# Kernel optimization log

Measured on AMD Instinct MI355X. Metric: run time of the kernel, lower is better.

The kernel has to match this reference:

```python
import jax, jax.numpy as jnp
import numpy as np

B, T, D, H, O, E, K = 2, 2048, 1024, 4096, 1024, 8, 2


def setup_inputs() -> dict:
    key = jax.random.key(0)
    ks = jax.random.split(key, 10)
    s = 0.02  # small init scale to keep activations well-conditioned
    return {
        "x": jax.random.normal(ks[0], (B, T, D), jnp.float32),
        "noise": jax.random.normal(ks[1], (B, T, E), jnp.float32),
        "Wg": jax.random.normal(ks[2], (D, E), jnp.float32) * s,
        "bg": jnp.zeros((E,), jnp.float32),
        "Wn": jax.random.normal(ks[3], (D, E), jnp.float32) * s,
        "bn": jnp.zeros((E,), jnp.float32),
        "W1": jax.random.normal(ks[4], (E, D, H), jnp.float32) * s,
        "b1": jnp.zeros((E, H), jnp.float32),
        "W2": jax.random.normal(ks[5], (E, H, O), jnp.float32) * s,
        "b2": jnp.zeros((E, O), jnp.float32),
    }


def reference(x, noise, Wg, bg, Wn, bn, W1, b1, W2, b2):
    # --- NoisyTopkRouter ---
    logits = x @ Wg + bg                    # [B,T,E]
    noise_logits = x @ Wn + bn              # [B,T,E]
    noisy = logits + noise * jax.nn.softplus(noise_logits)
    top_v, top_i = jax.lax.top_k(noisy, K)  # [B,T,K]
    # scatter top-k logits into a -inf background, softmax -> sparse gates
    mask = jax.nn.one_hot(top_i, E, dtype=noisy.dtype).sum(-2)  # [B,T,E] in {0,1}
    sparse_logits = jnp.where(mask > 0, noisy, -jnp.inf)
    gating = jax.nn.softmax(sparse_logits, axis=-1)
    # mask + L1 normalize (F.normalize p=1, dim=2)
    gating = gating * mask
    gating = gating / jnp.maximum(jnp.sum(jnp.abs(gating), axis=-1, keepdims=True), 1e-12)
    # --- dense run of ALL experts (faithful to the naive torch module) ---
    h = jax.nn.relu(jnp.einsum('btd,edh->beth', x, W1) + b1[:, None, :])   # [B,E,T,H]
    expert_out = jnp.einsum('beth,eho->beto', h, W2) + b2[:, None, :]       # [B,E,T,O]
    # combine: torch transposes to [B,T,E,O] then einsum 'bte,bteo->bto'
    out = jnp.einsum('bte,beto->bto', gating, expert_out)                   # [B,T,O]
    return out
```

## Files before the change

kernel.cpp:

```cpp
#include <hip/hip_runtime.h>
#include <hip/hip_bf16.h>

#define TOK 4096
#define DD  1024
#define HH  4096
#define OO  1024
#define EE  8
#define MAX_SLOTS 80

typedef float  f32x4  __attribute__((ext_vector_type(4)));
typedef __bf16 bf16x8 __attribute__((ext_vector_type(8)));
typedef __bf16 bf16x4 __attribute__((ext_vector_type(4)));
typedef unsigned int u32x4 __attribute__((ext_vector_type(4)));

union ABCast { u32x4 u; bf16x8 b; };

typedef __attribute__((address_space(3))) unsigned int       lds_uint;
typedef const __attribute__((address_space(1))) unsigned int glob_uint;

__device__ __forceinline__ void gload_lds16(void* lds, const void* g) {
    __builtin_amdgcn_global_load_lds((glob_uint*)g, (lds_uint*)lds, 16, 0, 0);
}

__global__ void router_kernel(const float* __restrict__ x, const float* __restrict__ noise,
                              const float* __restrict__ Wg, const float* __restrict__ bg,
                              const float* __restrict__ Wn, const float* __restrict__ bn,
                              int* __restrict__ topk_e, float* __restrict__ topk_g,
                              int* __restrict__ cnt)
{
    int wave = threadIdx.x >> 6;
    int lane = threadIdx.x & 63;
    int token = blockIdx.x * 4 + wave;
    const float* xr = x + (size_t)token * DD;
    float accg[EE], accn[EE];
#pragma unroll
    for (int e = 0; e < EE; ++e) { accg[e] = 0.f; accn[e] = 0.f; }
    for (int jj = 0; jj < DD / 64; ++jj) {
        int d = lane + jj * 64;
        float xv = xr[d];
        const float* wgr = Wg + d * EE;
        const float* wnr = Wn + d * EE;
#pragma unroll
        for (int e = 0; e < EE; ++e) {
            accg[e] += xv * wgr[e];
            accn[e] += xv * wnr[e];
        }
    }
#pragma unroll
    for (int off = 32; off; off >>= 1) {
#pragma unroll
        for (int e = 0; e < EE; ++e) {
            accg[e] += __shfl_down(accg[e], off, 64);
            accn[e] += __shfl_down(accn[e], off, 64);
        }
    }
    if (lane == 0) {
        float noisy[EE];
#pragma unroll
        for (int e = 0; e < EE; ++e) {
            float lg = accg[e] + bg[e];
            float nl = accn[e] + bn[e];
            float sp = fmaxf(nl, 0.f) + log1pf(expf(-fabsf(nl)));
            noisy[e] = lg + noise[(size_t)token * EE + e] * sp;
        }
        int i1 = 0; float v1 = noisy[0];
#pragma unroll
        for (int e = 1; e < EE; ++e) if (noisy[e] > v1) { v1 = noisy[e]; i1 = e; }
        int i2 = -1; float v2 = -1e30f;
#pragma unroll
        for (int e = 0; e < EE; ++e) if (e != i1 && noisy[e] > v2) { v2 = noisy[e]; i2 = e; }
        float ex = expf(v2 - v1);
        float g1 = 1.f / (1.f + ex);
        float g2 = ex / (1.f + ex);
        topk_e[token * 2] = i1;  topk_e[token * 2 + 1] = i2;
        topk_g[token * 2] = g1;  topk_g[token * 2 + 1] = g2;
        atomicAdd(&cnt[i1], 1);
        atomicAdd(&cnt[i2], 1);
    }
}

__global__ void plan_kernel(const int* __restrict__ cnt, int* __restrict__ base_row,
                            int* __restrict__ slot_e, int* __restrict__ slot_m,
                            int* __restrict__ fill)
{
    if (threadIdx.x == 0 && blockIdx.x == 0) {
        int s = 0;
        for (int e = 0; e < EE; ++e) {
            base_row[e] = s * 128;
            int tiles = (cnt[e] + 127) >> 7;
            for (int t = 0; t < tiles; ++t) { slot_e[s] = e; slot_m[s] = t; ++s; }
            fill[e] = 0;
        }
        for (int s2 = s; s2 < MAX_SLOTS; ++s2) { slot_e[s2] = -1; slot_m[s2] = 0; }
    }
}

__global__ void scatter_kernel(const int* __restrict__ topk_e, const float* __restrict__ topk_g,
                               const int* __restrict__ base_row, int* __restrict__ fill,
                               int* __restrict__ row_token, float* __restrict__ row_gate)
{
    int t = blockIdx.x * blockDim.x + threadIdx.x;
    if (t >= TOK * 2) return;
    int e = topk_e[t];
    int pos = atomicAdd(&fill[e], 1);
    int row = base_row[e] + pos;
    row_token[row] = t >> 1;
    row_gate[row] = topk_g[t];
}

__global__ void convert_x_kernel(const float* __restrict__ in, __bf16* __restrict__ out)
{
    int i = blockIdx.x * blockDim.x + threadIdx.x;
    f32x4 v = ((const f32x4*)in)[i];
    bf16x4 o;
    o.x = (__bf16)v.x; o.y = (__bf16)v.y; o.z = (__bf16)v.z; o.w = (__bf16)v.w;
    ((bf16x4*)out)[i] = o;
}

__global__ void transpose_cvt_kernel(const float* __restrict__ in, __bf16* __restrict__ out,
                                     int R, int C)
{
    __shared__ __bf16 tile[32][33];
    int e = blockIdx.z;
    const float* ine = in + (size_t)e * R * C;
    __bf16* oute = out + (size_t)e * R * C;
    int tx = threadIdx.x & 31, ty = threadIdx.x >> 5;
    int c0 = blockIdx.x * 32, r0 = blockIdx.y * 32;
#pragma unroll
    for (int i = 0; i < 4; ++i) {
        int r = r0 + ty + i * 8;
        tile[ty + i * 8][tx] = (__bf16)ine[(size_t)r * C + c0 + tx];
    }
    __syncthreads();
#pragma unroll
    for (int i = 0; i < 4; ++i) {
        int c = c0 + ty + i * 8;
        oute[(size_t)c * R + r0 + tx] = tile[tx][ty + i * 8];
    }
}

__global__ void gemm1_kernel(const __bf16* __restrict__ xb,
                             const __bf16* __restrict__ W1t,
                             const float* __restrict__ b1bias,
                             const int* __restrict__ slot_e, const int* __restrict__ slot_m,
                             const int* __restrict__ base_row, const int* __restrict__ cnt,
                             const int* __restrict__ row_token,
                             __bf16* __restrict__ h)
{
    int slot = blockIdx.y;
    int e = slot_e[slot];
    if (e < 0) return;
    int mt = slot_m[slot];
    int row0 = base_row[e] + mt * 128;
    int rows_in = min(128, cnt[e] - mt * 128);
    int n0 = blockIdx.x * 128;

    __shared__ u32x4 Alds[512];
    __shared__ u32x4 Blds[512];

    int tid = threadIdx.x;
    int wv = tid >> 6, lane = tid & 63;

    int ar0 = tid & 127,        ak0 = tid >> 7;
    int ar1 = ar0,              ak1 = ak0 + 2;
    int tok0 = (ar0 < rows_in) ? row_token[row0 + ar0] : 0;
    const char* ag0 = (const char*)(xb + (size_t)tok0 * DD + ak0 * 8);
    const char* ag1 = (const char*)(xb + (size_t)tok0 * DD + ak1 * 8);
    const __bf16* bbase = W1t + (size_t)e * HH * DD + (size_t)n0 * DD;
    const char* bg0 = (const char*)(bbase + (size_t)ar0 * DD + ak0 * 8);
    const char* bg1 = (const char*)(bbase + (size_t)ar1 * DD + ak1 * 8);

    int wm = wv & 1, wn = wv >> 1;
    int quad = lane >> 4, l16 = lane & 15;

    f32x4 acc[4][4];
#pragma unroll
    for (int i = 0; i < 4; ++i)
#pragma unroll
        for (int j = 0; j < 4; ++j) acc[i][j] = (f32x4)(0.0f);

    for (int kb = 0; kb < DD * 2; kb += 64) {
        __syncthreads();
        gload_lds16(&Alds[wv * 64],       ag0 + kb);
        gload_lds16(&Alds[256 + wv * 64], ag1 + kb);
        gload_lds16(&Blds[wv * 64],       bg0 + kb);
        gload_lds16(&Blds[256 + wv * 64], bg1 + kb);
        __syncthreads();
        ABCast af[4], bfr[4];
#pragma unroll
        for (int mf = 0; mf < 4; ++mf) af[mf].u = Alds[quad * 128 + wm * 64 + mf * 16 + l16];
#pragma unroll
        for (int nf = 0; nf < 4; ++nf) bfr[nf].u = Blds[quad * 128 + wn * 64 + nf * 16 + l16];
#pragma unroll
        for (int mf = 0; mf < 4; ++mf)
#pragma unroll
            for (int nf = 0; nf < 4; ++nf)
                acc[mf][nf] = __builtin_amdgcn_mfma_f32_16x16x32_bf16(af[mf].b, bfr[nf].b, acc[mf][nf], 0, 0, 0);
    }

#pragma unroll
    for (int mf = 0; mf < 4; ++mf) {
        int rl = wm * 64 + mf * 16 + quad * 4;
#pragma unroll
        for (int i = 0; i < 4; ++i) {
            int rli = rl + i;
            if (rli < rows_in) {
                size_t hrow = (size_t)(row0 + rli) * HH;
#pragma unroll
                for (int nf = 0; nf < 4; ++nf) {
                    int col = n0 + wn * 64 + nf * 16 + l16;
                    float v = acc[mf][nf][i] + b1bias[e * HH + col];
                    v = fmaxf(v, 0.f);
                    h[hrow + col] = (__bf16)v;
                }
            }
        }
    }
}

__global__ void gemm2_kernel(const __bf16* __restrict__ h,
                             const __bf16* __restrict__ W2t,
                             const float* __restrict__ b2bias,
                             const int* __restrict__ slot_e, const int* __restrict__ slot_m,
                             const int* __restrict__ base_row, const int* __restrict__ cnt,
                             const int* __restrict__ row_token, const float* __restrict__ row_gate,
                             float* __restrict__ out)
{
    int slot = blockIdx.y;
    int e = slot_e[slot];
    if (e < 0) return;
    int mt = slot_m[slot];
    int row0 = base_row[e] + mt * 128;
    int rows_in = min(128, cnt[e] - mt * 128);
    int n0 = blockIdx.x * 128;
    int kz = blockIdx.z;

    __shared__ u32x4 Alds[512];
    __shared__ u32x4 Blds[512];

    int tid = threadIdx.x;
    int wv = tid >> 6, lane = tid & 63;

    int ar0 = tid & 127, ak0 = tid >> 7;
    int ak1 = ak0 + 2;
    const char* ag0 = (const char*)(h + (size_t)(row0 + ar0) * HH + ak0 * 8);
    const char* ag1 = (const char*)(h + (size_t)(row0 + ar0) * HH + ak1 * 8);
    const __bf16* bbase = W2t + (size_t)e * OO * HH + (size_t)n0 * HH;
    const char* bg0 = (const char*)(bbase + (size_t)ar0 * HH + ak0 * 8);
    const char* bg1 = (const char*)(bbase + (size_t)ar0 * HH + ak1 * 8);

    int wm = wv & 1, wn = wv >> 1;
    int quad = lane >> 4, l16 = lane & 15;

    f32x4 acc[4][4];
#pragma unroll
    for (int i = 0; i < 4; ++i)
#pragma unroll
        for (int j = 0; j < 4; ++j) acc[i][j] = (f32x4)(0.0f);

    int kb0 = kz * 4096;
    for (int kb = kb0; kb < kb0 + 4096; kb += 64) {
        __syncthreads();
        gload_lds16(&Alds[wv * 64],       ag0 + kb);
        gload_lds16(&Alds[256 + wv * 64], ag1 + kb);
        gload_lds16(&Blds[wv * 64],       bg0 + kb);
        gload_lds16(&Blds[256 + wv * 64], bg1 + kb);
        __syncthreads();
        ABCast af[4], bfr[4];
#pragma unroll
        for (int mf = 0; mf < 4; ++mf) af[mf].u = Alds[quad * 128 + wm * 64 + mf * 16 + l16];
#pragma unroll
        for (int nf = 0; nf < 4; ++nf) bfr[nf].u = Blds[quad * 128 + wn * 64 + nf * 16 + l16];
#pragma unroll
        for (int mf = 0; mf < 4; ++mf)
#pragma unroll
            for (int nf = 0; nf < 4; ++nf)
                acc[mf][nf] = __builtin_amdgcn_mfma_f32_16x16x32_bf16(af[mf].b, bfr[nf].b, acc[mf][nf], 0, 0, 0);
    }

#pragma unroll
    for (int mf = 0; mf < 4; ++mf) {
        int rl = wm * 64 + mf * 16 + quad * 4;
#pragma unroll
        for (int i = 0; i < 4; ++i) {
            int rli = rl + i;
            if (rli < rows_in) {
                int token = row_token[row0 + rli];
                float gate = row_gate[row0 + rli];
                float* orow = out + (size_t)token * OO;
#pragma unroll
                for (int nf = 0; nf < 4; ++nf) {
                    int col = n0 + wn * 64 + nf * 16 + l16;
                    float v = acc[mf][nf][i];
                    if (kz == 0) v += b2bias[e * OO + col];
                    atomicAdd(&orow[col], gate * v);
                }
            }
        }
    }
}

extern "C" void kernel_launch(void* const* d_in, const int* in_sizes, int n_in,
                              void* d_out, int out_size, void* d_ws, size_t ws_size,
                              hipStream_t stream)
{
    const float* x     = (const float*)d_in[0];
    const float* noise = (const float*)d_in[1];
    const float* Wg    = (const float*)d_in[2];
    const float* bg    = (const float*)d_in[3];
    const float* Wn    = (const float*)d_in[4];
    const float* bn    = (const float*)d_in[5];
    const float* W1    = (const float*)d_in[6];
    const float* b1    = (const float*)d_in[7];
    const float* W2    = (const float*)d_in[8];
    const float* b2    = (const float*)d_in[9];
    float* out = (float*)d_out;

    char* p = (char*)d_ws;
    auto alloc = [&](size_t bytes) { char* r = p; p += (bytes + 255) & ~(size_t)255; return r; };
    __bf16* xb   = (__bf16*)alloc((size_t)TOK * DD * 2);
    __bf16* W1t  = (__bf16*)alloc((size_t)EE * DD * HH * 2);
    __bf16* W2t  = (__bf16*)alloc((size_t)EE * HH * OO * 2);
    __bf16* hbuf = (__bf16*)alloc((size_t)MAX_SLOTS * 128 * HH * 2);
    int*   topk_e    = (int*)alloc((size_t)TOK * 2 * 4);
    float* topk_g    = (float*)alloc((size_t)TOK * 2 * 4);
    int*   row_token = (int*)alloc((size_t)MAX_SLOTS * 128 * 4);
    float* row_gate  = (float*)alloc((size_t)MAX_SLOTS * 128 * 4);
    int*   cnt       = (int*)alloc(EE * 4);
    int*   fill      = (int*)alloc(EE * 4);
    int*   base_row  = (int*)alloc(EE * 4);
    int*   slot_e    = (int*)alloc(MAX_SLOTS * 4);
    int*   slot_m    = (int*)alloc(MAX_SLOTS * 4);

    hipMemsetAsync(out, 0, (size_t)out_size * 4, stream);
    hipMemsetAsync(cnt, 0, EE * 4, stream);

    router_kernel<<<TOK / 4, 256, 0, stream>>>(x, noise, Wg, bg, Wn, bn, topk_e, topk_g, cnt);
    plan_kernel<<<1, 64, 0, stream>>>(cnt, base_row, slot_e, slot_m, fill);
    scatter_kernel<<<(TOK * 2) / 256, 256, 0, stream>>>(topk_e, topk_g, base_row, fill, row_token, row_gate);
    convert_x_kernel<<<(TOK * DD / 4) / 256, 256, 0, stream>>>(x, xb);
    transpose_cvt_kernel<<<dim3(HH / 32, DD / 32, EE), 256, 0, stream>>>(W1, W1t, DD, HH);
    transpose_cvt_kernel<<<dim3(OO / 32, HH / 32, EE), 256, 0, stream>>>(W2, W2t, HH, OO);
    gemm1_kernel<<<dim3(HH / 128, MAX_SLOTS), 256, 0, stream>>>(xb, W1t, b1, slot_e, slot_m,
                                                                base_row, cnt, row_token, hbuf);
    gemm2_kernel<<<dim3(OO / 128, MAX_SLOTS, 2), 256, 0, stream>>>(hbuf, W2t, b2, slot_e, slot_m,
                                                                   base_row, cnt, row_token, row_gate, out);
}
```

Baseline: 902.8 us.

## Remap expert slots for XCD locality, swizzle LDS layout, vectorize weight transpose

Replaces the dense slot list with a fixed per-expert slot grid plus an overflow region. The GEMM blocks now use a 1D launch whose lowest index bits select the expert, so blocks for the same expert's weights share an XCD/L2 under round-robin dispatch. The LDS tiles for both GEMMs are reorganized row-major with an XOR swizzle on the k-chunk to avoid bank conflicts on fragment reads. The weight transpose-convert uses 64x64 tiles with float4 loads and bf16x4 stores. In exchange, many blocks are launched for empty slots and exit immediately, and the slot bookkeeping becomes more complex.

```diff
diff --git a/kernel.cpp b/kernel.cpp
--- a/kernel.cpp
+++ b/kernel.cpp
@@ -6,7 +6,12 @@
 #define HH  4096
 #define OO  1024
 #define EE  8
-#define MAX_SLOTS 80
+
+#define TPE        16
+#define SLOT_STRUCT (EE * TPE)
+#define SLOT_OVF   64
+#define SLOT_TOTAL (SLOT_STRUCT + SLOT_OVF)
+#define MAX_ACTIVE 72
 
 typedef float  f32x4  __attribute__((ext_vector_type(4)));
 typedef __bf16 bf16x8 __attribute__((ext_vector_type(8)));
@@ -79,33 +84,44 @@
     }
 }
 
-__global__ void plan_kernel(const int* __restrict__ cnt, int* __restrict__ base_row,
-                            int* __restrict__ slot_e, int* __restrict__ slot_m,
+__global__ void plan_kernel(const int* __restrict__ cnt,
+                            int* __restrict__ s_e, int* __restrict__ s_rows,
+                            int* __restrict__ s_cbase, int* __restrict__ ov_base,
                             int* __restrict__ fill)
 {
     if (threadIdx.x == 0 && blockIdx.x == 0) {
-        int s = 0;
+        for (int s = 0; s < SLOT_TOTAL; ++s) { s_e[s] = -1; s_rows[s] = 0; s_cbase[s] = 0; }
+        int c = 0, ovn = 0;
         for (int e = 0; e < EE; ++e) {
-            base_row[e] = s * 128;
+            fill[e] = 0;
+            ov_base[e] = ovn;
             int tiles = (cnt[e] + 127) >> 7;
-            for (int t = 0; t < tiles; ++t) { slot_e[s] = e; slot_m[s] = t; ++s; }
-            fill[e] = 0;
-        }
-        for (int s2 = s; s2 < MAX_SLOTS; ++s2) { slot_e[s2] = -1; slot_m[s2] = 0; }
+            for (int t = 0; t < tiles; ++t) {
+                int slot = (t < TPE) ? (e * TPE + t) : (SLOT_STRUCT + ovn + (t - TPE));
+                s_e[slot] = e;
+                s_rows[slot] = min(128, cnt[e] - t * 128);
+                s_cbase[slot] = c * 128;
+                ++c;
+            }
+            if (tiles > TPE) ovn += tiles - TPE;
+        }
     }
 }
 
 __global__ void scatter_kernel(const int* __restrict__ topk_e, const float* __restrict__ topk_g,
-                               const int* __restrict__ base_row, int* __restrict__ fill,
+                               const int* __restrict__ s_cbase, const int* __restrict__ ov_base,
+                               int* __restrict__ fill,
                                int* __restrict__ row_token, float* __restrict__ row_gate)
 {
     int t = blockIdx.x * blockDim.x + threadIdx.x;
     if (t >= TOK * 2) return;
     int e = topk_e[t];
     int pos = atomicAdd(&fill[e], 1);
-    int row = base_row[e] + pos;
-    row_token[row] = t >> 1;
-    row_gate[row] = topk_g[t];
+    int tile = pos >> 7;
+    int slot = (tile < TPE) ? (e * TPE + tile) : (SLOT_STRUCT + ov_base[e] + (tile - TPE));
+    int crow = s_cbase[slot] + (pos & 127);
+    row_token[crow] = t >> 1;
+    row_gate[crow] = topk_g[t];
 }
 
 __global__ void convert_x_kernel(const float* __restrict__ in, __bf16* __restrict__ out)
@@ -120,40 +136,55 @@
 __global__ void transpose_cvt_kernel(const float* __restrict__ in, __bf16* __restrict__ out,
                                      int R, int C)
 {
-    __shared__ __bf16 tile[32][33];
+    __shared__ __bf16 tile[64 * 68];
     int e = blockIdx.z;
     const float* ine = in + (size_t)e * R * C;
     __bf16* oute = out + (size_t)e * R * C;
-    int tx = threadIdx.x & 31, ty = threadIdx.x >> 5;
-    int c0 = blockIdx.x * 32, r0 = blockIdx.y * 32;
+    int c0 = blockIdx.x * 64, r0 = blockIdx.y * 64;
+    int tx = threadIdx.x & 15, ty = threadIdx.x >> 4;
 #pragma unroll
     for (int i = 0; i < 4; ++i) {
-        int r = r0 + ty + i * 8;
-        tile[ty + i * 8][tx] = (__bf16)ine[(size_t)r * C + c0 + tx];
+        int r = ty + i * 16;
+        f32x4 v = *(const f32x4*)&ine[(size_t)(r0 + r) * C + c0 + tx * 4];
+        tile[(4 * tx + 0) * 68 + r] = (__bf16)v.x;
+        tile[(4 * tx + 1) * 68 + r] = (__bf16)v.y;
+        tile[(4 * tx + 2) * 68 + r] = (__bf16)v.z;
+        tile[(4 * tx + 3) * 68 + r] = (__bf16)v.w;
     }
     __syncthreads();
-#pragma unroll
-    for (int i = 0; i < 4; ++i) {
-        int c = c0 + ty + i * 8;
-        oute[(size_t)c * R + r0 + tx] = tile[tx][ty + i * 8];
+    int c = threadIdx.x >> 2, q = threadIdx.x & 3;
+#pragma unroll
+    for (int it = 0; it < 4; ++it) {
+        int r4 = q * 4 + it * 16;
+        bf16x4 vv = *(const bf16x4*)&tile[c * 68 + r4];
+        *(bf16x4*)&oute[(size_t)(c0 + c) * R + r0 + r4] = vv;
     }
 }
 
 __global__ void gemm1_kernel(const __bf16* __restrict__ xb,
                              const __bf16* __restrict__ W1t,
                              const float* __restrict__ b1bias,
-                             const int* __restrict__ slot_e, const int* __restrict__ slot_m,
-                             const int* __restrict__ base_row, const int* __restrict__ cnt,
+                             const int* __restrict__ s_e, const int* __restrict__ s_rows,
+                             const int* __restrict__ s_cbase,
                              const int* __restrict__ row_token,
                              __bf16* __restrict__ h)
 {
-    int slot = blockIdx.y;
-    int e = slot_e[slot];
+    int lin = blockIdx.x;
+    int slot, nt;
+    if (lin < EE * TPE * (HH / 128)) {
+        int eb = lin & 7, r = lin >> 3;
+        slot = eb * TPE + (r & 15);
+        nt = r >> 4;
+    } else {
+        int idx = lin - EE * TPE * (HH / 128);
+        nt = idx & 31;
+        slot = SLOT_STRUCT + (idx >> 5);
+    }
+    int e = s_e[slot];
     if (e < 0) return;
-    int mt = slot_m[slot];
-    int row0 = base_row[e] + mt * 128;
-    int rows_in = min(128, cnt[e] - mt * 128);
-    int n0 = blockIdx.x * 128;
+    int rows_in = s_rows[slot];
+    int cb = s_cbase[slot];
+    int n0 = nt * 128;
 
     __shared__ u32x4 Alds[512];
     __shared__ u32x4 Blds[512];
@@ -161,17 +192,18 @@
     int tid = threadIdx.x;
     int wv = tid >> 6, lane = tid & 63;
 
-    int ar0 = tid & 127,        ak0 = tid >> 7;
-    int ar1 = ar0,              ak1 = ak0 + 2;
-    int tok0 = (ar0 < rows_in) ? row_token[row0 + ar0] : 0;
-    const char* ag0 = (const char*)(xb + (size_t)tok0 * DD + ak0 * 8);
-    const char* ag1 = (const char*)(xb + (size_t)tok0 * DD + ak1 * 8);
-    const __bf16* bbase = W1t + (size_t)e * HH * DD + (size_t)n0 * DD;
-    const char* bg0 = (const char*)(bbase + (size_t)ar0 * DD + ak0 * 8);
-    const char* bg1 = (const char*)(bbase + (size_t)ar1 * DD + ak1 * 8);
+    int row0 = tid >> 2;
+    int kc0 = (tid & 3) ^ ((tid >> 3) & 3);
+    int tok0 = (row0 < rows_in) ? row_token[cb + row0] : 0;
+    int tok1 = (row0 + 64 < rows_in) ? row_token[cb + row0 + 64] : 0;
+    const char* ag0 = (const char*)xb + ((size_t)tok0 * DD + kc0 * 8) * 2;
+    const char* ag1 = (const char*)xb + ((size_t)tok1 * DD + kc0 * 8) * 2;
+    const char* bg0 = (const char*)W1t + ((size_t)e * HH * DD + (size_t)(n0 + row0) * DD + kc0 * 8) * 2;
+    const char* bg1 = bg0 + (size_t)64 * DD * 2;
 
     int wm = wv & 1, wn = wv >> 1;
     int quad = lane >> 4, l16 = lane & 15;
+    int swz = quad ^ ((l16 >> 1) & 3);
 
     f32x4 acc[4][4];
 #pragma unroll
@@ -188,9 +220,9 @@
         __syncthreads();
         ABCast af[4], bfr[4];
 #pragma unroll
-        for (int mf = 0; mf < 4; ++mf) af[mf].u = Alds[quad * 128 + wm * 64 + mf * 16 + l16];
-#pragma unroll
-        for (int nf = 0; nf < 4; ++nf) bfr[nf].u = Blds[quad * 128 + wn * 64 + nf * 16 + l16];
+        for (int mf = 0; mf < 4; ++mf) af[mf].u = Alds[(wm * 64 + mf * 16 + l16) * 4 + swz];
+#pragma unroll
+        for (int nf = 0; nf < 4; ++nf) bfr[nf].u = Blds[(wn * 64 + nf * 16 + l16) * 4 + swz];
 #pragma unroll
         for (int mf = 0; mf < 4; ++mf)
 #pragma unroll
@@ -205,7 +237,7 @@
         for (int i = 0; i < 4; ++i) {
             int rli = rl + i;
             if (rli < rows_in) {
-                size_t hrow = (size_t)(row0 + rli) * HH;
+                size_t hrow = (size_t)(cb + rli) * HH;
 #pragma unroll
                 for (int nf = 0; nf < 4; ++nf) {
                     int col = n0 + wn * 64 + nf * 16 + l16;
@@ -221,19 +253,30 @@
 __global__ void gemm2_kernel(const __bf16* __restrict__ h,
                              const __bf16* __restrict__ W2t,
                              const float* __restrict__ b2bias,
-                             const int* __restrict__ slot_e, const int* __restrict__ slot_m,
-                             const int* __restrict__ base_row, const int* __restrict__ cnt,
+                             const int* __restrict__ s_e, const int* __restrict__ s_rows,
+                             const int* __restrict__ s_cbase,
                              const int* __restrict__ row_token, const float* __restrict__ row_gate,
                              float* __restrict__ out)
 {
-    int slot = blockIdx.y;
-    int e = slot_e[slot];
+    int lin = blockIdx.x;
+    int slot, nt, kz;
+    if (lin < EE * TPE * (OO / 128) * 2) {
+        int eb = lin & 7, r = lin >> 3;
+        slot = eb * TPE + (r & 15);
+        int r2 = r >> 4;
+        nt = r2 & 7;
+        kz = r2 >> 3;
+    } else {
+        int idx = lin - EE * TPE * (OO / 128) * 2;
+        nt = idx & 7;
+        kz = (idx >> 3) & 1;
+        slot = SLOT_STRUCT + (idx >> 4);
+    }
+    int e = s_e[slot];
     if (e < 0) return;
-    int mt = slot_m[slot];
-    int row0 = base_row[e] + mt * 128;
-    int rows_in = min(128, cnt[e] - mt * 128);
-    int n0 = blockIdx.x * 128;
-    int kz = blockIdx.z;
+    int rows_in = s_rows[slot];
+    int cb = s_cbase[slot];
+    int n0 = nt * 128;
 
     __shared__ u32x4 Alds[512];
     __shared__ u32x4 Blds[512];
@@ -241,16 +284,16 @@
     int tid = threadIdx.x;
     int wv = tid >> 6, lane = tid & 63;
 
-    int ar0 = tid & 127, ak0 = tid >> 7;
-    int ak1 = ak0 + 2;
-    const char* ag0 = (const char*)(h + (size_t)(row0 + ar0) * HH + ak0 * 8);
-    const char* ag1 = (const char*)(h + (size_t)(row0 + ar0) * HH + ak1 * 8);
-    const __bf16* bbase = W2t + (size_t)e * OO * HH + (size_t)n0 * HH;
-    const char* bg0 = (const char*)(bbase + (size_t)ar0 * HH + ak0 * 8);
-    const char* bg1 = (const char*)(bbase + (size_t)ar0 * HH + ak1 * 8);
+    int row0 = tid >> 2;
+    int kc0 = (tid & 3) ^ ((tid >> 3) & 3);
+    const char* ag0 = (const char*)h + ((size_t)(cb + row0) * HH + kc0 * 8) * 2;
+    const char* ag1 = ag0 + (size_t)64 * HH * 2;
+    const char* bg0 = (const char*)W2t + ((size_t)e * OO * HH + (size_t)(n0 + row0) * HH + kc0 * 8) * 2;
+    const char* bg1 = bg0 + (size_t)64 * HH * 2;
 
     int wm = wv & 1, wn = wv >> 1;
     int quad = lane >> 4, l16 = lane & 15;
+    int swz = quad ^ ((l16 >> 1) & 3);
 
     f32x4 acc[4][4];
 #pragma unroll
@@ -268,9 +311,9 @@
         __syncthreads();
         ABCast af[4], bfr[4];
 #pragma unroll
-        for (int mf = 0; mf < 4; ++mf) af[mf].u = Alds[quad * 128 + wm * 64 + mf * 16 + l16];
-#pragma unroll
-        for (int nf = 0; nf < 4; ++nf) bfr[nf].u = Blds[quad * 128 + wn * 64 + nf * 16 + l16];
+        for (int mf = 0; mf < 4; ++mf) af[mf].u = Alds[(wm * 64 + mf * 16 + l16) * 4 + swz];
+#pragma unroll
+        for (int nf = 0; nf < 4; ++nf) bfr[nf].u = Blds[(wn * 64 + nf * 16 + l16) * 4 + swz];
 #pragma unroll
         for (int mf = 0; mf < 4; ++mf)
 #pragma unroll
@@ -285,8 +328,8 @@
         for (int i = 0; i < 4; ++i) {
             int rli = rl + i;
             if (rli < rows_in) {
-                int token = row_token[row0 + rli];
-                float gate = row_gate[row0 + rli];
+                int token = row_token[cb + rli];
+                float gate = row_gate[cb + rli];
                 float* orow = out + (size_t)token * OO;
 #pragma unroll
                 for (int nf = 0; nf < 4; ++nf) {
@@ -321,28 +364,32 @@
     __bf16* xb   = (__bf16*)alloc((size_t)TOK * DD * 2);
     __bf16* W1t  = (__bf16*)alloc((size_t)EE * DD * HH * 2);
     __bf16* W2t  = (__bf16*)alloc((size_t)EE * HH * OO * 2);
-    __bf16* hbuf = (__bf16*)alloc((size_t)MAX_SLOTS * 128 * HH * 2);
+    __bf16* hbuf = (__bf16*)alloc((size_t)MAX_ACTIVE * 128 * HH * 2);
     int*   topk_e    = (int*)alloc((size_t)TOK * 2 * 4);
     float* topk_g    = (float*)alloc((size_t)TOK * 2 * 4);
-    int*   row_token = (int*)alloc((size_t)MAX_SLOTS * 128 * 4);
-    float* row_gate  = (float*)alloc((size_t)MAX_SLOTS * 128 * 4);
+    int*   row_token = (int*)alloc((size_t)MAX_ACTIVE * 128 * 4);
+    float* row_gate  = (float*)alloc((size_t)MAX_ACTIVE * 128 * 4);
     int*   cnt       = (int*)alloc(EE * 4);
     int*   fill      = (int*)alloc(EE * 4);
-    int*   base_row  = (int*)alloc(EE * 4);
-    int*   slot_e    = (int*)alloc(MAX_SLOTS * 4);
-    int*   slot_m    = (int*)alloc(MAX_SLOTS * 4);
+    int*   ov_base   = (int*)alloc(EE * 4);
+    int*   s_e       = (int*)alloc(SLOT_TOTAL * 4);
+    int*   s_rows    = (int*)alloc(SLOT_TOTAL * 4);
+    int*   s_cbase   = (int*)alloc(SLOT_TOTAL * 4);
 
     hipMemsetAsync(out, 0, (size_t)out_size * 4, stream);
     hipMemsetAsync(cnt, 0, EE * 4, stream);
 
     router_kernel<<<TOK / 4, 256, 0, stream>>>(x, noise, Wg, bg, Wn, bn, topk_e, topk_g, cnt);
-    plan_kernel<<<1, 64, 0, stream>>>(cnt, base_row, slot_e, slot_m, fill);
-    scatter_kernel<<<(TOK * 2) / 256, 256, 0, stream>>>(topk_e, topk_g, base_row, fill, row_token, row_gate);
+    plan_kernel<<<1, 64, 0, stream>>>(cnt, s_e, s_rows, s_cbase, ov_base, fill);
+    scatter_kernel<<<(TOK * 2) / 256, 256, 0, stream>>>(topk_e, topk_g, s_cbase, ov_base, fill,
+                                                        row_token, row_gate);
     convert_x_kernel<<<(TOK * DD / 4) / 256, 256, 0, stream>>>(x, xb);
-    transpose_cvt_kernel<<<dim3(HH / 32, DD / 32, EE), 256, 0, stream>>>(W1, W1t, DD, HH);
-    transpose_cvt_kernel<<<dim3(OO / 32, HH / 32, EE), 256, 0, stream>>>(W2, W2t, HH, OO);
-    gemm1_kernel<<<dim3(HH / 128, MAX_SLOTS), 256, 0, stream>>>(xb, W1t, b1, slot_e, slot_m,
-                                                                base_row, cnt, row_token, hbuf);
-    gemm2_kernel<<<dim3(OO / 128, MAX_SLOTS, 2), 256, 0, stream>>>(hbuf, W2t, b2, slot_e, slot_m,
-                                                                   base_row, cnt, row_token, row_gate, out);
-}
+    transpose_cvt_kernel<<<dim3(HH / 64, DD / 64, EE), 256, 0, stream>>>(W1, W1t, DD, HH);
+    transpose_cvt_kernel<<<dim3(OO / 64, HH / 64, EE), 256, 0, stream>>>(W2, W2t, HH, OO);
+
+    int g1_blocks = EE * TPE * (HH / 128) + SLOT_OVF * (HH / 128);
+    gemm1_kernel<<<g1_blocks, 256, 0, stream>>>(xb, W1t, b1, s_e, s_rows, s_cbase, row_token, hbuf);
+    int g2_blocks = EE * TPE * (OO / 128) * 2 + SLOT_OVF * (OO / 128) * 2;
+    gemm2_kernel<<<g2_blocks, 256, 0, stream>>>(hbuf, W2t, b2, s_e, s_rows, s_cbase,
+                                                row_token, row_gate, out);
+}
```

Result: faster. 750.5 us (-16.9%).
